# Kernel tuning notes

Hardware: AMD Instinct MI355X
Metric: run time of the kernel (lower is better)

## Reference

```python
import jax, jax.numpy as jnp
import numpy as np

B, N, F, T, K, O = 64, 34, 16, 96, 3, 64
EPS = 1e-8  # torch cosine_similarity eps


def _laplacian(A):
    # get_L_d: normalized graph Laplacian L = I - D^{-1/2} A D^{-1/2}
    n = A.shape[-1]
    d = A.sum(-1)                                   # (..., N) row-sum degrees
    dinv = jnp.where(d > 0, jax.lax.rsqrt(jnp.maximum(d, 1e-12)), 0.0)
    I = jnp.eye(n, dtype=A.dtype)
    return I - dinv[..., :, None] * A * dinv[..., None, :]


def _dynamic_adjacency(gs, position, distance):
    # gs: (B,T,N,F); uses features [1:3] as 2-d wind vector
    v = gs[..., 1:3]                                # (B,T,N,2)
    vn = jnp.linalg.norm(v, axis=-1)                # (B,T,N)
    pn = jnp.linalg.norm(position, axis=-1)         # (N,)
    dots = jnp.einsum('btnc,mc->btnm', v, position)  # (B,T,N,N)
    cos = dots / (jnp.maximum(vn, EPS)[..., None] * jnp.maximum(pn, EPS))
    cos = jnp.maximum(cos, 0.0)                     # cosine_sims[cos<=0]=0
    A = cos * vn[..., None] / distance              # wind_speed / distance
    # F.normalize(p=2, dim=(1,2)): per-sample Frobenius normalization
    frob = jnp.sqrt(jnp.sum(A * A, axis=(-2, -1), keepdims=True))
    return A / jnp.maximum(frob, 1e-12)


def setup_inputs() -> dict:
    key = jax.random.key(0)
    ks = jax.random.split(key, 6)
    x = jax.random.normal(ks[0], (B, N, F, T), jnp.float32)
    st_attention = jax.random.normal(ks[1], (B, K, N, N), jnp.float32)
    position = jax.random.normal(ks[2], (N, 2), jnp.float32)
    distance = jax.random.uniform(ks[3], (N, N), jnp.float32, 1.0, 10.0)
    Theta = jax.random.normal(ks[4], (K, F, O), jnp.float32) * 0.1
    Theta_L = jax.random.normal(ks[5], (K, F, O), jnp.float32) * 0.1
    return {"x": x, "st_attention": st_attention, "position": position,
            "distance": distance, "Theta": Theta, "Theta_L": Theta_L}


def reference(x, st_attention, position, distance, Theta, Theta_L):
    Kk = Theta.shape[0]
    gs = jnp.transpose(x, (0, 3, 1, 2))             # (B,T,N,F) -- vectorize over timesteps
    A = _dynamic_adjacency(gs, position, distance)  # (B,T,N,N)
    L1 = _laplacian(A)
    L2 = _laplacian(jnp.swapaxes(A, -1, -2))
    n = A.shape[-1]
    I = jnp.broadcast_to(jnp.eye(n, dtype=A.dtype), L1.shape)
    cheb1, cheb2 = [I, L1], [I, L2]
    for i in range(2, Kk):
        cheb1.append(2.0 * jnp.matmul(L1, cheb1[-1]) - cheb1[-2])
        cheb2.append(2.0 * jnp.matmul(L2, cheb2[-1]) - cheb2[-2])
    # softmax over dim=1 of (B,N,N) slice -> axis 2 of (B,K,N,N)
    att = jax.nn.softmax(st_attention, axis=2)      # (B,K,N,N)
    out = jnp.zeros(gs.shape[:3] + (Theta.shape[-1],), dtype=x.dtype)  # (B,T,N,O)
    for k in range(Kk):
        a = att[:, k][:, None]                       # (B,1,N,N) broadcast over T
        Tk1 = cheb1[k] * a
        Tk2 = cheb2[k] * a
        # T_k_with_att^T @ graph_signal @ theta
        out = out + jnp.einsum('btij,btif,fo->btjo', Tk1, gs, Theta[k]) \
                  + jnp.einsum('btij,btif,fo->btjo', Tk2, gs, Theta_L[k])
    out = jax.nn.relu(out)
    return jnp.transpose(out, (0, 2, 3, 1))          # (B,N,O,T)
```

## Files before the change

### kernel.cpp

```cpp
#include <hip/hip_runtime.h>
#include <cstddef>

namespace {
constexpr int cB = 64, cN = 34, cF = 16, cT = 96, cK = 3, cO = 64;
constexpr int LP = 72;
constexpr int HPA = 80;
constexpr int BHP = 88;
constexpr int T4 = cT / 4;
constexpr float cEPS = 1e-8f;

typedef __attribute__((ext_vector_type(8))) _Float16 f16x8;
typedef __attribute__((ext_vector_type(8))) short   s16x8;
typedef __attribute__((ext_vector_type(4))) float   f32x4;

__device__ inline unsigned short f2h(float v) {
    _Float16 h = (_Float16)v;
    return __builtin_bit_cast(unsigned short, h);
}
__device__ inline float h2f(unsigned short u) {
    return (float)__builtin_bit_cast(_Float16, u);
}

__device__ inline size_t hstage_idx(int b, int t4, int j, int s) {
    return (((size_t)b * cN + j) * cO + (s >> 2)) * cT + 4 * t4 + (s & 3);
}
}

__global__ __launch_bounds__(256) void att_softmax_k(const float* __restrict__ st,
                                                     float* __restrict__ att) {
    int idx = blockIdx.x * blockDim.x + threadIdx.x;
    if (idx >= cB * cK * cN) return;
    int j = idx % cN;
    int bk = idx / cN;
    const float* base = st + (size_t)bk * cN * cN + j;
    float v[cN];
    float m = -3.402823466e38f;
#pragma unroll
    for (int i = 0; i < cN; ++i) { v[i] = base[(size_t)i * cN]; m = fmaxf(m, v[i]); }
    float s = 0.f;
#pragma unroll
    for (int i = 0; i < cN; ++i) { v[i] = __expf(v[i] - m); s += v[i]; }
    float inv = 1.f / s;
    float* ob = att + (size_t)bk * cN * cN + j;
#pragma unroll
    for (int i = 0; i < cN; ++i) ob[(size_t)i * cN] = v[i] * inv;
}

__global__ __launch_bounds__(256, 4) void cheb_h_k(
    const float* __restrict__ x,
    const float* __restrict__ att,
    const float* __restrict__ pos,
    const float* __restrict__ dist,
    unsigned* __restrict__ Hst)
{
    __shared__ __align__(16) unsigned short s_L1[cN * LP];
    __shared__ __align__(16) unsigned short s_L2[cN * LP];
    __shared__ __align__(16) unsigned short s_M1T[cN * LP];
    __shared__ __align__(16) unsigned short s_M3T[cN * LP];
    __shared__ __align__(16) unsigned short s_gsT[cF * LP];
    __shared__ __align__(16) unsigned short s_H[cN * HPA];
    __shared__ float s_d0[cN], s_v1[cN], s_v2[cN], s_p1[cN], s_p2[cN], s_di1[cN], s_di2[cN];

    const int tid = threadIdx.x;
    const int lane = tid & 63;
    const int w = tid >> 6;
    const int lr = lane & 15;
    const int lg = lane >> 4;
    const int kb8 = lg * 8;

    const unsigned g = blockIdx.x;
    const unsigned lin = (g & 7u) * (cB * cT / 8) + (g >> 3);
    const int b = lin / cT, t = lin % cT;

    for (int i2 = tid; i2 < cN * LP / 2; i2 += 256) {
        ((unsigned*)s_L1)[i2] = 0u; ((unsigned*)s_L2)[i2] = 0u;
        ((unsigned*)s_M1T)[i2] = 0u; ((unsigned*)s_M3T)[i2] = 0u;
    }
    if (tid < cN) {
        float px = pos[2 * tid], py = pos[2 * tid + 1];
        float pn = sqrtf(px * px + py * py);
        float r = 1.f / fmaxf(pn, cEPS);
        s_p1[tid] = px * r; s_p2[tid] = py * r;
        s_d0[tid] = att[((size_t)b * cK) * cN * cN + tid * cN + tid];
    } else if (tid >= 64 && tid < 64 + cN) {
        int n = tid - 64;
        float x1 = x[(((size_t)b * cN + n) * cF + 1) * cT + t];
        float x2 = x[(((size_t)b * cN + n) * cF + 2) * cT + t];
        float vn = sqrtf(x1 * x1 + x2 * x2);
        float s = vn / fmaxf(vn, cEPS);
        s_v1[n] = x1 * s; s_v2[n] = x2 * s;
    }
    for (int idx = tid; idx < cF * LP; idx += 256) {
        int f = idx / LP, n = idx - f * LP;
        unsigned short v = 0;
        if (n < cN) v = f2h(x[(((size_t)b * cN + n) * cF + f) * cT + t]);
        s_gsT[idx] = v;
    }
    __syncthreads();

    float* Af = (float*)s_L1;
#pragma unroll
    for (int e = 0; e < 5; ++e) {
        int idx = tid + 256 * e;
        if (idx < cN * cN) {
            int i = idx / cN, m = idx - i * cN;
            float dot = s_v1[i] * s_p1[m] + s_v2[i] * s_p2[m];
            Af[idx] = __fdividef(fmaxf(dot, 0.f), dist[idx]);
        }
    }
    __syncthreads();

    if (tid < cN) {
        float s = 0.f;
#pragma unroll
        for (int m = 0; m < cN; ++m) s += Af[tid * cN + m];
        s_di1[tid] = (s > 0.f) ? rsqrtf(fmaxf(s, 1e-12f)) : 0.f;
    } else if (tid >= 64 && tid < 64 + cN) {
        int j = tid - 64;
        float s = 0.f;
#pragma unroll
        for (int i = 0; i < cN; ++i) s += Af[i * cN + j];
        s_di2[j] = (s > 0.f) ? rsqrtf(fmaxf(s, 1e-12f)) : 0.f;
    }
    float aij[5], aji[5];
#pragma unroll
    for (int e = 0; e < 5; ++e) {
        int idx = tid + 256 * e;
        if (idx < cN * cN) {
            int i = idx / cN, j = idx - i * cN;
            aij[e] = Af[idx];
            aji[e] = Af[j * cN + i];
        }
    }
    __syncthreads();

    const float* att1 = att + ((size_t)b * cK + 1) * cN * cN;
    const float* att2 = att + ((size_t)b * cK + 2) * cN * cN;
#pragma unroll
    for (int e = 0; e < 5; ++e) {
        int idx = tid + 256 * e;
        if (idx < cN * cN) {
            int i = idx / cN, j = idx - i * cN;
            float diag = (i == j) ? 1.f : 0.f;
            float l1 = diag - s_di1[i] * aij[e] * s_di1[j];
            float l2 = diag - s_di2[i] * aji[e] * s_di2[j];
            int rm = i * LP + j, tm = j * LP + i;
            s_L1[rm] = f2h(l1);
            s_L1[rm + cN] = 0;
            if (j < 4) s_L1[i * LP + 68 + j] = 0;
            s_L2[rm] = f2h(l2);
            float a1 = att1[idx];
            s_M1T[tm] = f2h(a1 * l1);
            s_M3T[tm] = f2h(a1 * l2);
        }
    }
    __syncthreads();

    const unsigned short* Ah = (w < 2) ? s_L1 : s_L2;
    const int nnt = (w & 1) ? 1 : 2;
    const int ntb0 = (w & 1) ? 32 : 0;
    f32x4 cd0[3], cd1[3];
#pragma unroll
    for (int mt = 0; mt < 3; ++mt) {
        cd0[mt] = (f32x4){0.f, 0.f, 0.f, 0.f};
        cd1[mt] = (f32x4){0.f, 0.f, 0.f, 0.f};
    }
#pragma unroll
    for (int ks = 0; ks < 2; ++ks) {
        f16x8 fah[3];
#pragma unroll
        for (int mt = 0; mt < 3; ++mt)
            fah[mt] = *(const f16x8*)&Ah[(mt * 16 + lr) * LP + 32 * ks + kb8];
#pragma unroll
        for (int un = 0; un < 2; ++un) {
            if (un == 1 && nnt < 2) break;
            int col = ntb0 + un * 16 + lr;
            s16x8 fbb;
#pragma unroll
            for (int e2 = 0; e2 < 8; ++e2) {
                int kk = 32 * ks + kb8 + e2;
                fbb[e2] = (kk < cN) ? (short)Ah[kk * LP + col] : (short)0;
            }
            f16x8 fb = __builtin_bit_cast(f16x8, fbb);
#pragma unroll
            for (int mt = 0; mt < 3; ++mt) {
                f32x4 acc = un ? cd1[mt] : cd0[mt];
                acc = __builtin_amdgcn_mfma_f32_16x16x32_f16(fah[mt], fb, acc, 0, 0, 0);
                if (un) cd1[mt] = acc; else cd0[mt] = acc;
            }
        }
    }
    __syncthreads();

    {
        unsigned short* Md = (w < 2) ? s_L1 : s_L2;
#pragma unroll
        for (int un = 0; un < 2; ++un) {
            if (un == 1 && nnt < 2) break;
            int jb = ntb0 + un * 16 + lr;
            if (jb < cN) {
#pragma unroll
                for (int mt = 0; mt < 3; ++mt) {
#pragma unroll
                    for (int r = 0; r < 4; ++r) {
                        int i = mt * 16 + lg * 4 + r;
                        if (i < cN) {
                            float dv = un ? cd1[mt][r] : cd0[mt][r];
                            float cv = 2.f * dv - ((i == jb) ? 1.f : 0.f);
                            Md[jb * LP + i] = f2h(att2[i * cN + jb] * cv);
                        }
                    }
                }
            }
        }
    }
    __syncthreads();

    {
        const unsigned short* Ap = (w == 0) ? s_M1T : (w == 1) ? s_L1
                                 : (w == 2) ? s_M3T : s_L2;
        f32x4 hd[3];
#pragma unroll
        for (int mt = 0; mt < 3; ++mt) hd[mt] = (f32x4){0.f, 0.f, 0.f, 0.f};
#pragma unroll
        for (int ks = 0; ks < 2; ++ks) {
            f16x8 fb = *(const f16x8*)&s_gsT[lr * LP + 32 * ks + kb8];
#pragma unroll
            for (int mt = 0; mt < 3; ++mt) {
                f16x8 fa = *(const f16x8*)&Ap[(mt * 16 + lr) * LP + 32 * ks + kb8];
                hd[mt] = __builtin_amdgcn_mfma_f32_16x16x32_f16(fa, fb, hd[mt], 0, 0, 0);
            }
        }
        int pc = 16 * (w + 1);
#pragma unroll
        for (int mt = 0; mt < 3; ++mt) {
#pragma unroll
            for (int r = 0; r < 4; ++r) {
                int j = mt * 16 + lg * 4 + r;
                if (j < cN) s_H[j * HPA + pc + lr] = f2h(hd[mt][r]);
            }
        }
    }
    for (int idx = tid; idx < cN * cF; idx += 256) {
        int j = idx >> 4, f = idx & 15;
        s_H[j * HPA + f] = f2h(s_d0[j] * h2f(s_gsT[f * LP + j]));
    }
    __syncthreads();

    {
        const unsigned* src = (const unsigned*)s_H;
        const int t4 = t >> 2, tt = t & 3;
        for (int i2 = tid; i2 < cN * (HPA / 2); i2 += 256) {
            int j = i2 / (HPA / 2), c = i2 - j * (HPA / 2);
            Hst[hstage_idx(b, t4, j, tt * 40 + c)] = src[i2];
        }
    }
}

__global__ __launch_bounds__(256, 4) void proj_k(
    const unsigned* __restrict__ Hst,
    const float* __restrict__ Th,
    const float* __restrict__ ThL,
    float* __restrict__ out)
{
    __shared__ __align__(16) unsigned short s_H[144 * BHP + 16];

    const int tid = threadIdx.x;
    const int lane = tid & 63;
    const int w = tid >> 6;
    const int lr = lane & 15;
    const int lg = lane >> 4;
    const int kb8 = lg * 8;
    const int ocol = w * 16 + lr;

    const unsigned g = blockIdx.x;
    const unsigned lin = (g & 7u) * (cB * T4 / 8) + (g >> 3);
    const int b = lin / T4, t4 = lin % T4;
    const int t0 = t4 * 4;

    f16x8 bfr[3];
#pragma unroll
    for (int s = 0; s < 3; ++s) {
#pragma unroll
        for (int j = 0; j < 8; ++j) {
            int cc = 32 * s + kb8 + j;
            float v = 0.f;
            if (cc < 80) {
                int p = cc >> 4, f = cc & 15;
                if (p == 0)      v = Th[f * cO + ocol] + ThL[f * cO + ocol];
                else if (p == 1) v = Th[(cF + f) * cO + ocol];
                else if (p == 2) v = Th[(2 * cF + f) * cO + ocol];
                else if (p == 3) v = ThL[(cF + f) * cO + ocol];
                else             v = ThL[(2 * cF + f) * cO + ocol];
            }
            bfr[s][j] = (_Float16)v;
        }
    }

    {
        unsigned* dst = (unsigned*)s_H;
        for (int i2 = tid; i2 < 144 * (BHP / 2); i2 += 256) {
            int r = i2 / (BHP / 2), c = i2 - r * (BHP / 2);
            unsigned v = 0u;
            if (r < 136 && c < 40) {
                int j = r >> 2, tt = r & 3;
                v = Hst[hstage_idx(b, t4, j, tt * 40 + c)];
            }
            dst[i2] = v;
        }
    }
    __syncthreads();

    f32x4 acc[9];
#pragma unroll
    for (int mt = 0; mt < 9; ++mt) acc[mt] = (f32x4){0.f, 0.f, 0.f, 0.f};
#pragma unroll
    for (int s = 0; s < 3; ++s) {
#pragma unroll
        for (int mt = 0; mt < 9; ++mt) {
            f16x8 a = *(const f16x8*)&s_H[(mt * 16 + lr) * BHP + kb8 + 32 * s];
            acc[mt] = __builtin_amdgcn_mfma_f32_16x16x32_f16(a, bfr[s], acc[mt], 0, 0, 0);
        }
    }

#pragma unroll
    for (int mt = 0; mt < 9; ++mt) {
        int j = 4 * mt + lg;
        if (j < cN) {
            float4 v;
            v.x = fmaxf(acc[mt][0], 0.f);
            v.y = fmaxf(acc[mt][1], 0.f);
            v.z = fmaxf(acc[mt][2], 0.f);
            v.w = fmaxf(acc[mt][3], 0.f);
            *(float4*)&out[(((size_t)b * cN + j) * cO + ocol) * cT + t0] = v;
        }
    }
}

extern "C" void kernel_launch(void* const* d_in, const int* in_sizes, int n_in,
                              void* d_out, int out_size, void* d_ws, size_t ws_size,
                              hipStream_t stream) {
    const float* x    = (const float*)d_in[0];
    const float* st   = (const float*)d_in[1];
    const float* pos  = (const float*)d_in[2];
    const float* dist = (const float*)d_in[3];
    const float* Th   = (const float*)d_in[4];
    const float* ThL  = (const float*)d_in[5];
    float* out = (float*)d_out;
    float* att = (float*)d_ws;
    unsigned* Hst = (unsigned*)d_out;

    att_softmax_k<<<(cB * cK * cN + 255) / 256, 256, 0, stream>>>(st, att);
    cheb_h_k<<<cB * cT, 256, 0, stream>>>(x, att, pos, dist, Hst);
    proj_k<<<cB * T4, 256, 0, stream>>>(Hst, Th, ThL, out);
}
```

Measured before the change: 97.38 us.

## Store transposed Laplacians, write H directly to global, drop staging buffer

Keeps explicitly transposed copies of L1 and L2 in shared memory so the B-operand of the Chebyshev MFMA loads as one vector instead of eight strided scalar reads. The H tile is no longer staged in shared memory: MFMA results are paired across lanes with a shuffle and written straight to global, which removes a barrier and a copy pass. It also pads the adjacency scratch to a stride of 36, splits the degree row and column sums across two threads each, shrinks the gsT pitch, and raises the occupancy hint to 5. In exchange it uses more shared memory and issues smaller, less coalesced global stores.

```diff
diff --git a/kernel.cpp b/kernel.cpp
--- a/kernel.cpp
+++ b/kernel.cpp
@@ -4,13 +4,12 @@
 namespace {
 constexpr int cB = 64, cN = 34, cF = 16, cT = 96, cK = 3, cO = 64;
 constexpr int LP = 72;
-constexpr int HPA = 80;
+constexpr int GP = 64;
 constexpr int BHP = 88;
 constexpr int T4 = cT / 4;
 constexpr float cEPS = 1e-8f;
 
 typedef __attribute__((ext_vector_type(8))) _Float16 f16x8;
-typedef __attribute__((ext_vector_type(8))) short   s16x8;
 typedef __attribute__((ext_vector_type(4))) float   f32x4;
 
 __device__ inline unsigned short f2h(float v) {
@@ -46,7 +45,7 @@
     for (int i = 0; i < cN; ++i) ob[(size_t)i * cN] = v[i] * inv;
 }
 
-__global__ __launch_bounds__(256, 4) void cheb_h_k(
+__global__ __launch_bounds__(256, 5) void cheb_h_k(
     const float* __restrict__ x,
     const float* __restrict__ att,
     const float* __restrict__ pos,
@@ -55,10 +54,11 @@
 {
     __shared__ __align__(16) unsigned short s_L1[cN * LP];
     __shared__ __align__(16) unsigned short s_L2[cN * LP];
+    __shared__ __align__(16) unsigned short s_LT1[cN * LP];
+    __shared__ __align__(16) unsigned short s_LT2[cN * LP];
     __shared__ __align__(16) unsigned short s_M1T[cN * LP];
     __shared__ __align__(16) unsigned short s_M3T[cN * LP];
-    __shared__ __align__(16) unsigned short s_gsT[cF * LP];
-    __shared__ __align__(16) unsigned short s_H[cN * HPA];
+    __shared__ __align__(16) unsigned short s_gsT[cF * GP];
     __shared__ float s_d0[cN], s_v1[cN], s_v2[cN], s_p1[cN], s_p2[cN], s_di1[cN], s_di2[cN];
 
     const int tid = threadIdx.x;
@@ -71,9 +71,11 @@
     const unsigned g = blockIdx.x;
     const unsigned lin = (g & 7u) * (cB * cT / 8) + (g >> 3);
     const int b = lin / cT, t = lin % cT;
+    const int t4 = t >> 2, tt = t & 3;
 
     for (int i2 = tid; i2 < cN * LP / 2; i2 += 256) {
         ((unsigned*)s_L1)[i2] = 0u; ((unsigned*)s_L2)[i2] = 0u;
+        ((unsigned*)s_LT1)[i2] = 0u; ((unsigned*)s_LT2)[i2] = 0u;
         ((unsigned*)s_M1T)[i2] = 0u; ((unsigned*)s_M3T)[i2] = 0u;
     }
     if (tid < cN) {
@@ -90,8 +92,8 @@
         float s = vn / fmaxf(vn, cEPS);
         s_v1[n] = x1 * s; s_v2[n] = x2 * s;
     }
-    for (int idx = tid; idx < cF * LP; idx += 256) {
-        int f = idx / LP, n = idx - f * LP;
+    for (int idx = tid; idx < cF * GP; idx += 256) {
+        int f = idx >> 6, n = idx & 63;
         unsigned short v = 0;
         if (n < cN) v = f2h(x[(((size_t)b * cN + n) * cF + f) * cT + t]);
         s_gsT[idx] = v;
@@ -105,22 +107,29 @@
         if (idx < cN * cN) {
             int i = idx / cN, m = idx - i * cN;
             float dot = s_v1[i] * s_p1[m] + s_v2[i] * s_p2[m];
-            Af[idx] = __fdividef(fmaxf(dot, 0.f), dist[idx]);
-        }
-    }
-    __syncthreads();
-
-    if (tid < cN) {
-        float s = 0.f;
-#pragma unroll
-        for (int m = 0; m < cN; ++m) s += Af[tid * cN + m];
-        s_di1[tid] = (s > 0.f) ? rsqrtf(fmaxf(s, 1e-12f)) : 0.f;
-    } else if (tid >= 64 && tid < 64 + cN) {
-        int j = tid - 64;
-        float s = 0.f;
-#pragma unroll
-        for (int i = 0; i < cN; ++i) s += Af[i * cN + j];
-        s_di2[j] = (s > 0.f) ? rsqrtf(fmaxf(s, 1e-12f)) : 0.f;
+            Af[i * 36 + m] = __fdividef(fmaxf(dot, 0.f), dist[idx]);
+        }
+    }
+    __syncthreads();
+
+    if (tid < 136) {
+        int s = tid >> 1, half = tid & 1;
+        float acc = 0.f;
+        if (s < cN) {
+            const float* row = Af + s * 36 + half * 17;
+#pragma unroll
+            for (int m = 0; m < 17; ++m) acc += row[m];
+        } else {
+            int j = s - cN;
+            const float* col = Af + half * 17 * 36 + j;
+#pragma unroll
+            for (int i = 0; i < 17; ++i) acc += col[i * 36];
+        }
+        float tot = acc + __shfl_xor(acc, 1, 64);
+        if (half == 0) {
+            float d = (tot > 0.f) ? rsqrtf(fmaxf(tot, 1e-12f)) : 0.f;
+            if (s < cN) s_di1[s] = d; else s_di2[s - cN] = d;
+        }
     }
     float aij[5], aji[5];
 #pragma unroll
@@ -128,8 +137,8 @@
         int idx = tid + 256 * e;
         if (idx < cN * cN) {
             int i = idx / cN, j = idx - i * cN;
-            aij[e] = Af[idx];
-            aji[e] = Af[j * cN + i];
+            aij[e] = Af[i * 36 + j];
+            aji[e] = Af[j * 36 + i];
         }
     }
     __syncthreads();
@@ -144,11 +153,14 @@
             float diag = (i == j) ? 1.f : 0.f;
             float l1 = diag - s_di1[i] * aij[e] * s_di1[j];
             float l2 = diag - s_di2[i] * aji[e] * s_di2[j];
+            unsigned short h1 = f2h(l1), h2b = f2h(l2);
             int rm = i * LP + j, tm = j * LP + i;
-            s_L1[rm] = f2h(l1);
+            s_L1[rm] = h1;
             s_L1[rm + cN] = 0;
             if (j < 4) s_L1[i * LP + 68 + j] = 0;
-            s_L2[rm] = f2h(l2);
+            s_L2[rm] = h2b;
+            s_LT1[tm] = h1;
+            s_LT2[tm] = h2b;
             float a1 = att1[idx];
             s_M1T[tm] = f2h(a1 * l1);
             s_M3T[tm] = f2h(a1 * l2);
@@ -157,6 +169,7 @@
     __syncthreads();
 
     const unsigned short* Ah = (w < 2) ? s_L1 : s_L2;
+    const unsigned short* At = (w < 2) ? s_LT1 : s_LT2;
     const int nnt = (w & 1) ? 1 : 2;
     const int ntb0 = (w & 1) ? 32 : 0;
     f32x4 cd0[3], cd1[3];
@@ -175,13 +188,7 @@
         for (int un = 0; un < 2; ++un) {
             if (un == 1 && nnt < 2) break;
             int col = ntb0 + un * 16 + lr;
-            s16x8 fbb;
-#pragma unroll
-            for (int e2 = 0; e2 < 8; ++e2) {
-                int kk = 32 * ks + kb8 + e2;
-                fbb[e2] = (kk < cN) ? (short)Ah[kk * LP + col] : (short)0;
-            }
-            f16x8 fb = __builtin_bit_cast(f16x8, fbb);
+            f16x8 fb = *(const f16x8*)&At[col * LP + 32 * ks + kb8];
 #pragma unroll
             for (int mt = 0; mt < 3; ++mt) {
                 f32x4 acc = un ? cd1[mt] : cd0[mt];
@@ -224,35 +231,35 @@
         for (int mt = 0; mt < 3; ++mt) hd[mt] = (f32x4){0.f, 0.f, 0.f, 0.f};
 #pragma unroll
         for (int ks = 0; ks < 2; ++ks) {
-            f16x8 fb = *(const f16x8*)&s_gsT[lr * LP + 32 * ks + kb8];
+            f16x8 fb = *(const f16x8*)&s_gsT[lr * GP + 32 * ks + kb8];
 #pragma unroll
             for (int mt = 0; mt < 3; ++mt) {
                 f16x8 fa = *(const f16x8*)&Ap[(mt * 16 + lr) * LP + 32 * ks + kb8];
                 hd[mt] = __builtin_amdgcn_mfma_f32_16x16x32_f16(fa, fb, hd[mt], 0, 0, 0);
             }
         }
-        int pc = 16 * (w + 1);
+        for (int idx = tid; idx < cN * 8; idx += 256) {
+            int j = idx >> 3, c = idx & 7;
+            float d = s_d0[j];
+            unsigned short lo = f2h(d * h2f(s_gsT[(2 * c) * GP + j]));
+            unsigned short hi = f2h(d * h2f(s_gsT[(2 * c + 1) * GP + j]));
+            Hst[hstage_idx(b, t4, j, tt * 40 + c)] = (unsigned)lo | ((unsigned)hi << 16);
+        }
+        const int pc = 16 * (w + 1);
+        const int cdw = (pc >> 1) + (lr >> 1);
 #pragma unroll
         for (int mt = 0; mt < 3; ++mt) {
 #pragma unroll
             for (int r = 0; r < 4; ++r) {
                 int j = mt * 16 + lg * 4 + r;
-                if (j < cN) s_H[j * HPA + pc + lr] = f2h(hd[mt][r]);
-            }
-        }
-    }
-    for (int idx = tid; idx < cN * cF; idx += 256) {
-        int j = idx >> 4, f = idx & 15;
-        s_H[j * HPA + f] = f2h(s_d0[j] * h2f(s_gsT[f * LP + j]));
-    }
-    __syncthreads();
-
-    {
-        const unsigned* src = (const unsigned*)s_H;
-        const int t4 = t >> 2, tt = t & 3;
-        for (int i2 = tid; i2 < cN * (HPA / 2); i2 += 256) {
-            int j = i2 / (HPA / 2), c = i2 - j * (HPA / 2);
-            Hst[hstage_idx(b, t4, j, tt * 40 + c)] = src[i2];
+                unsigned mine = (unsigned)f2h(hd[mt][r]);
+                unsigned other = __shfl_xor(mine, 1, 64);
+                unsigned dword = (lr & 1) ? ((other & 0xffffu) | (mine << 16))
+                                          : (mine | (other << 16));
+                bool mystore = ((lr & 1) == 0) ? (r < 2) : (r >= 2);
+                if (mystore && j < cN)
+                    Hst[hstage_idx(b, t4, j, tt * 40 + cdw)] = dword;
+            }
         }
     }
 }
```

Result: slower. 105.9 us (+8.8%).

## Write Chebyshev H tiles straight to global, dropping the shared staging buffer

Applied to the files above, without the earlier changes.

Removes the s_H shared-memory staging tile and its extra barrier. MFMA results are now packed into half2 dwords with a lane shuffle and stored directly to the global Hst buffer, and the degree-scaled identity term is also written directly. Shared zeroing is vectorized to 16-byte stores, Md writes are packed two halves per dword, and launch bounds are raised from 4 to 6 blocks per CU to exploit the lower LDS footprint. The trade-off is more, less coalesced global stores and possible register pressure from the tighter occupancy target.

```diff
diff --git a/kernel.cpp b/kernel.cpp
--- a/kernel.cpp
+++ b/kernel.cpp
@@ -4,7 +4,6 @@
 namespace {
 constexpr int cB = 64, cN = 34, cF = 16, cT = 96, cK = 3, cO = 64;
 constexpr int LP = 72;
-constexpr int HPA = 80;
 constexpr int BHP = 88;
 constexpr int T4 = cT / 4;
 constexpr float cEPS = 1e-8f;
@@ -46,7 +45,7 @@
     for (int i = 0; i < cN; ++i) ob[(size_t)i * cN] = v[i] * inv;
 }
 
-__global__ __launch_bounds__(256, 4) void cheb_h_k(
+__global__ __launch_bounds__(256, 6) void cheb_h_k(
     const float* __restrict__ x,
     const float* __restrict__ att,
     const float* __restrict__ pos,
@@ -58,7 +57,6 @@
     __shared__ __align__(16) unsigned short s_M1T[cN * LP];
     __shared__ __align__(16) unsigned short s_M3T[cN * LP];
     __shared__ __align__(16) unsigned short s_gsT[cF * LP];
-    __shared__ __align__(16) unsigned short s_H[cN * HPA];
     __shared__ float s_d0[cN], s_v1[cN], s_v2[cN], s_p1[cN], s_p2[cN], s_di1[cN], s_di2[cN];
 
     const int tid = threadIdx.x;
@@ -71,10 +69,14 @@
     const unsigned g = blockIdx.x;
     const unsigned lin = (g & 7u) * (cB * cT / 8) + (g >> 3);
     const int b = lin / cT, t = lin % cT;
-
-    for (int i2 = tid; i2 < cN * LP / 2; i2 += 256) {
-        ((unsigned*)s_L1)[i2] = 0u; ((unsigned*)s_L2)[i2] = 0u;
-        ((unsigned*)s_M1T)[i2] = 0u; ((unsigned*)s_M3T)[i2] = 0u;
+    const int t4 = t >> 2, tt = t & 3;
+
+    {
+        f32x4 z = (f32x4){0.f, 0.f, 0.f, 0.f};
+        for (int i2 = tid; i2 < cN * LP / 8; i2 += 256) {
+            ((f32x4*)s_L1)[i2] = z; ((f32x4*)s_L2)[i2] = z;
+            ((f32x4*)s_M1T)[i2] = z; ((f32x4*)s_M3T)[i2] = z;
+        }
     }
     if (tid < cN) {
         float px = pos[2 * tid], py = pos[2 * tid + 1];
@@ -202,12 +204,18 @@
 #pragma unroll
                 for (int mt = 0; mt < 3; ++mt) {
 #pragma unroll
-                    for (int r = 0; r < 4; ++r) {
-                        int i = mt * 16 + lg * 4 + r;
-                        if (i < cN) {
-                            float dv = un ? cd1[mt][r] : cd0[mt][r];
-                            float cv = 2.f * dv - ((i == jb) ? 1.f : 0.f);
-                            Md[jb * LP + i] = f2h(att2[i * cN + jb] * cv);
+                    for (int h = 0; h < 2; ++h) {
+                        int ia = mt * 16 + lg * 4 + 2 * h;
+                        if (ia < cN) {
+                            float dva = h ? (un ? cd1[mt][2] : cd0[mt][2])
+                                          : (un ? cd1[mt][0] : cd0[mt][0]);
+                            float dvb = h ? (un ? cd1[mt][3] : cd0[mt][3])
+                                          : (un ? cd1[mt][1] : cd0[mt][1]);
+                            float cva = 2.f * dva - ((ia == jb) ? 1.f : 0.f);
+                            float cvb = 2.f * dvb - ((ia + 1 == jb) ? 1.f : 0.f);
+                            unsigned lo = f2h(att2[ia * cN + jb] * cva);
+                            unsigned hi = f2h(att2[(ia + 1) * cN + jb] * cvb);
+                            ((unsigned*)Md)[(jb * LP + ia) >> 1] = lo | (hi << 16);
                         }
                     }
                 }
@@ -231,28 +239,28 @@
                 hd[mt] = __builtin_amdgcn_mfma_f32_16x16x32_f16(fa, fb, hd[mt], 0, 0, 0);
             }
         }
-        int pc = 16 * (w + 1);
+        for (int idx = tid; idx < cN * 8; idx += 256) {
+            int j = idx >> 3, c = idx & 7;
+            float d = s_d0[j];
+            unsigned lo = f2h(d * h2f(s_gsT[(2 * c) * LP + j]));
+            unsigned hi = f2h(d * h2f(s_gsT[(2 * c + 1) * LP + j]));
+            Hst[hstage_idx(b, t4, j, tt * 40 + c)] = lo | (hi << 16);
+        }
+        const int pc = 16 * (w + 1);
+        const int cdw = (pc >> 1) + (lr >> 1);
 #pragma unroll
         for (int mt = 0; mt < 3; ++mt) {
 #pragma unroll
             for (int r = 0; r < 4; ++r) {
                 int j = mt * 16 + lg * 4 + r;
-                if (j < cN) s_H[j * HPA + pc + lr] = f2h(hd[mt][r]);
-            }
-        }
-    }
-    for (int idx = tid; idx < cN * cF; idx += 256) {
-        int j = idx >> 4, f = idx & 15;
-        s_H[j * HPA + f] = f2h(s_d0[j] * h2f(s_gsT[f * LP + j]));
-    }
-    __syncthreads();
-
-    {
-        const unsigned* src = (const unsigned*)s_H;
-        const int t4 = t >> 2, tt = t & 3;
-        for (int i2 = tid; i2 < cN * (HPA / 2); i2 += 256) {
-            int j = i2 / (HPA / 2), c = i2 - j * (HPA / 2);
-            Hst[hstage_idx(b, t4, j, tt * 40 + c)] = src[i2];
+                unsigned mine = (unsigned)f2h(hd[mt][r]);
+                unsigned other = __shfl_xor(mine, 1, 64);
+                unsigned dword = (lr & 1) ? ((other & 0xffffu) | (mine << 16))
+                                          : (mine | (other << 16));
+                bool mystore = ((lr & 1) == 0) ? (r < 2) : (r >= 2);
+                if (mystore && j < cN)
+                    Hst[hstage_idx(b, t4, j, tt * 40 + cdw)] = dword;
+            }
         }
     }
 }
```

After: 90.96 us. 1.07x faster.
